# Optimization experiments

Hardware: AMD Instinct MI355X
Metric: run time of the kernel (lower is better)

The kernel has to match this reference:

```python
import jax, jax.numpy as jnp
import numpy as np

N_NODES = 50000
N_EDGES = 800000
IN_DIM = 128
HID = 32
HEADS = 4
OUT_DIM = 128
NEG_SLOPE = 0.2


def setup_inputs() -> dict:
    key = jax.random.key(0)
    ks = jax.random.split(key, 10)
    s = lambda fan_in: 1.0 / np.sqrt(fan_in)
    return {
        "x": jax.random.normal(ks[0], (N_NODES, IN_DIM), dtype=jnp.float32),
        "edge_index": jax.random.randint(ks[1], (2, N_EDGES), 0, N_NODES, dtype=jnp.int64),
        # encoder GATConv: in=IN_DIM, out=HID, heads=HEADS (concat)
        "W1": jax.random.normal(ks[2], (IN_DIM, HEADS * HID), dtype=jnp.float32) * s(IN_DIM),
        "att_src1": jax.random.normal(ks[3], (HEADS, HID), dtype=jnp.float32) * s(HID),
        "att_dst1": jax.random.normal(ks[4], (HEADS, HID), dtype=jnp.float32) * s(HID),
        "b1": jnp.zeros((HEADS * HID,), dtype=jnp.float32),
        # decoder GATConv: in=HEADS*HID, out=OUT_DIM, heads=1
        "W2": jax.random.normal(ks[5], (HEADS * HID, OUT_DIM), dtype=jnp.float32) * s(HEADS * HID),
        "att_src2": jax.random.normal(ks[6], (1, OUT_DIM), dtype=jnp.float32) * s(OUT_DIM),
        "att_dst2": jax.random.normal(ks[7], (1, OUT_DIM), dtype=jnp.float32) * s(OUT_DIM),
        "b2": jnp.zeros((OUT_DIM,), dtype=jnp.float32),
    }


def _gat_conv(x, src, dst, W, att_src, att_dst, bias, heads, out_ch):
    """PyG-style GATConv (v1), eval mode (dropout off), self-loops already in src/dst."""
    n = x.shape[0]
    h = (x @ W).reshape(n, heads, out_ch)                 # [N,H,C]
    a_src = jnp.einsum("nhc,hc->nh", h, att_src)          # [N,H]
    a_dst = jnp.einsum("nhc,hc->nh", h, att_dst)          # [N,H]
    e = jax.nn.leaky_relu(a_src[src] + a_dst[dst], NEG_SLOPE)  # [E,H]
    # segment softmax over destination neighborhoods
    e_max = jax.ops.segment_max(e, dst, num_segments=n)   # [N,H]
    e_exp = jnp.exp(e - e_max[dst])
    denom = jax.ops.segment_sum(e_exp, dst, num_segments=n)
    alpha = e_exp / (denom[dst] + 1e-16)                  # [E,H]
    msg = h[src] * alpha[:, :, None]                      # [E,H,C]
    out = jax.ops.segment_sum(msg, dst, num_segments=n)   # [N,H,C]
    return out.reshape(n, heads * out_ch) + bias


def reference(x, edge_index, W1, att_src1, att_dst1, b1, W2, att_src2, att_dst2, b2):
    n = x.shape[0]
    loops = jnp.arange(n, dtype=edge_index.dtype)
    src = jnp.concatenate([edge_index[0], loops])
    dst = jnp.concatenate([edge_index[1], loops])
    z = jax.nn.relu(_gat_conv(x, src, dst, W1, att_src1, att_dst1, b1, HEADS, HID))
    x_hat = jax.nn.relu(_gat_conv(z, src, dst, W2, att_src2, att_dst2, b2, 1, OUT_DIM))
    return x_hat
```

## Files before the change

### kernel.cpp

```cpp
#include <hip/hip_runtime.h>
#include <hip/hip_bf16.h>
#include <cstddef>

#define N_NODES 50000
#define N_EDGES_RAW 800000
#define E_TOT (N_EDGES_RAW + N_NODES)
#define DIM 128
#define NEG_SLOPE 0.2f

#define NBUCK 196
#define CHUNK 4096
#define NBLK_E ((E_TOT + CHUNK - 1) / CHUNK)

typedef __attribute__((ext_vector_type(8))) short bf16x8;
typedef __attribute__((ext_vector_type(4))) float f32x4;

__device__ __forceinline__ ushort f2bf(float f) {
  unsigned u = __float_as_uint(f);
  return (ushort)((u + 0x7FFFu + ((u >> 16) & 1u)) >> 16);
}

__device__ __forceinline__ void get_edge(const int* __restrict__ ei, int is64,
                                         int e, int& s, int& d) {
  if (e >= N_EDGES_RAW) { s = e - N_EDGES_RAW; d = s; return; }
  if (is64) {
    s = ei[2 * (size_t)e];
    d = ei[2 * ((size_t)N_EDGES_RAW + (size_t)e)];
  } else {
    s = ei[e];
    d = ei[N_EDGES_RAW + e];
  }
}

__device__ __forceinline__ int detect_inline(const int* __restrict__ ei,
                                             int* sflag) {
  const int t = threadIdx.x;
  if (t < 64) {
    int hi = ei[2 * t + 1];
    unsigned long long b = __ballot(hi != 0);
    if (t == 0) *sflag = (b == 0ULL) ? 1 : 0;
  }
  __syncthreads();
  return *sflag;
}

__device__ __forceinline__ void prep_one(const float* __restrict__ w,
                                         const float* __restrict__ atts,
                                         const float* __restrict__ attd,
                                         ushort* __restrict__ wtx,
                                         int H, int idx) {
  const int c = idx >> 7, k = idx & 127;
  const int C = 128 / H;
  float v;
  if (c < 128) {
    v = w[k * 128 + c];
  } else if (c < 128 + H) {
    const int hd = c - 128;
    float s = 0.f;
    for (int j = 0; j < C; ++j) s += w[k * 128 + hd * C + j] * atts[hd * C + j];
    v = s;
  } else if (c < 128 + 2 * H) {
    const int hd = c - 128 - H;
    float s = 0.f;
    for (int j = 0; j < C; ++j) s += w[k * 128 + hd * C + j] * attd[hd * C + j];
    v = s;
  } else {
    v = 0.f;
  }
  wtx[idx] = f2bf(v);
}

__global__ __launch_bounds__(256) void setup(const float* __restrict__ W1,
                                             const float* __restrict__ as1,
                                             const float* __restrict__ ad1,
                                             ushort* __restrict__ wtx1,
                                             const float* __restrict__ W2,
                                             const float* __restrict__ as2,
                                             const float* __restrict__ ad2,
                                             ushort* __restrict__ wtx2,
                                             int* __restrict__ gbcnt) {
  const int b = blockIdx.x, t = threadIdx.x;
  if (b < 72) {
    prep_one(W1, as1, ad1, wtx1, 4, b * 256 + t);
  } else if (b < 144) {
    prep_one(W2, as2, ad2, wtx2, 1, (b - 72) * 256 + t);
  } else {
    if (t < NBUCK) gbcnt[t] = 0;
  }
}

__global__ __launch_bounds__(256) void bucket_count(const int* __restrict__ ei,
                                                    int* __restrict__ gbcnt) {
  __shared__ int hist[NBUCK];
  __shared__ int sflag;
  const int t = threadIdx.x;
  if (t < NBUCK) hist[t] = 0;
  const int is64 = detect_inline(ei, &sflag);
  __syncthreads();
  const int e0 = blockIdx.x * CHUNK;
#pragma unroll
  for (int i = 0; i < CHUNK / 256; ++i) {
    int e = e0 + i * 256 + t;
    if (e < E_TOT) {
      int s, d;
      get_edge(ei, is64, e, s, d);
      atomicAdd(&hist[d >> 8], 1);
    }
  }
  __syncthreads();
  if (t < NBUCK && hist[t] > 0) atomicAdd(&gbcnt[t], hist[t]);
}

__global__ __launch_bounds__(256) void bucket_scan(const int* __restrict__ gbcnt,
                                                   int* __restrict__ bstart,
                                                   int* __restrict__ gcur) {
  __shared__ int wtot[4];
  const int t = threadIdx.x, lane = t & 63, wid = t >> 6;
  int v = (t < NBUCK) ? gbcnt[t] : 0;
  int sc = v;
#pragma unroll
  for (int m = 1; m < 64; m <<= 1) {
    int o = __shfl_up(sc, m, 64);
    if (lane >= m) sc += o;
  }
  if (lane == 63) wtot[wid] = sc;
  __syncthreads();
  int off = 0;
  for (int w = 0; w < wid; ++w) off += wtot[w];
  int excl = off + sc - v;
  if (t < NBUCK) {
    bstart[t] = excl;
    gcur[t] = excl;
  }
  if (t == 255) bstart[NBUCK] = off + sc;
}

__global__ __launch_bounds__(256) void bucket_scatter(const int* __restrict__ ei,
                                                      int* __restrict__ gcur,
                                                      unsigned* __restrict__ tmp) {
  __shared__ int hist[NBUCK];
  __shared__ int base[NBUCK];
  __shared__ int sflag;
  const int t = threadIdx.x;
  if (t < NBUCK) hist[t] = 0;
  const int is64 = detect_inline(ei, &sflag);
  __syncthreads();
  const int e0 = blockIdx.x * CHUNK;
  unsigned pair[CHUNK / 256];
  int rank[CHUNK / 256];
#pragma unroll
  for (int i = 0; i < CHUNK / 256; ++i) {
    int e = e0 + i * 256 + t;
    if (e < E_TOT) {
      int s, d;
      get_edge(ei, is64, e, s, d);
      pair[i] = (unsigned)s | ((unsigned)d << 16);
      rank[i] = atomicAdd(&hist[d >> 8], 1);
    }
  }
  __syncthreads();
  if (t < NBUCK && hist[t] > 0) base[t] = atomicAdd(&gcur[t], hist[t]);
  __syncthreads();
#pragma unroll
  for (int i = 0; i < CHUNK / 256; ++i) {
    int e = e0 + i * 256 + t;
    if (e < E_TOT) {
      int b = (int)(pair[i] >> 24);
      tmp[base[b] + rank[i]] = pair[i];
    }
  }
}

__global__ __launch_bounds__(256) void bucket_sort(const unsigned* __restrict__ tmp,
                                                   const int* __restrict__ bstart,
                                                   int* __restrict__ csr_src,
                                                   int* __restrict__ rp,
                                                   int* __restrict__ deg) {
  __shared__ int cnt[256];
  __shared__ int cur[256];
  __shared__ int wtot[4];
  const int b = blockIdx.x;
  const int t = threadIdx.x, lane = t & 63, wid = t >> 6;
  const int p0 = bstart[b], p1 = bstart[b + 1];
  cnt[t] = 0;
  __syncthreads();
  for (int j = p0 + t; j < p1; j += 256) {
    unsigned pr = tmp[j];
    atomicAdd(&cnt[(pr >> 16) & 255u], 1);
  }
  __syncthreads();
  int v = cnt[t];
  int sc = v;
#pragma unroll
  for (int m = 1; m < 64; m <<= 1) {
    int o = __shfl_up(sc, m, 64);
    if (lane >= m) sc += o;
  }
  if (lane == 63) wtot[wid] = sc;
  __syncthreads();
  int off = 0;
  for (int w = 0; w < wid; ++w) off += wtot[w];
  const int excl = off + sc - v;
  const int node = b * 256 + t;
  if (node < N_NODES) {
    deg[node] = v;
    rp[node] = p0 + excl;
  }
  cur[t] = excl;
  __syncthreads();
  for (int j = p0 + t; j < p1; j += 256) {
    unsigned pr = tmp[j];
    int ld = (int)((pr >> 16) & 255u);
    int r = atomicAdd(&cur[ld], 1);
    csr_src[p0 + r] = (int)(pr & 0xFFFFu);
  }
}

template <int H>
__global__ __launch_bounds__(256) void gemm_att(const float* __restrict__ in,
                                                const ushort* __restrict__ wtx,
                                                ushort* __restrict__ h_bf,
                                                float* __restrict__ a_src,
                                                float* __restrict__ a_dst) {
  const int wid = threadIdx.x >> 6;
  const int lane = threadIdx.x & 63;
  const int tile = blockIdx.x * 4 + wid;
  if (tile >= N_NODES / 16) return;
  const int row0 = tile * 16;
  const int rA = lane & 15;
  const int g = lane >> 4;

  f32x4 acc[9];
#pragma unroll
  for (int ct = 0; ct < 9; ++ct) acc[ct] = (f32x4){0.f, 0.f, 0.f, 0.f};

#pragma unroll
  for (int ks = 0; ks < 4; ++ks) {
    const int k0 = ks * 32 + g * 8;
    const float* ap = in + (size_t)(row0 + rA) * DIM + k0;
    float4 a0 = *(const float4*)ap;
    float4 a1 = *(const float4*)(ap + 4);
    bf16x8 af;
    af[0] = (short)f2bf(a0.x); af[1] = (short)f2bf(a0.y);
    af[2] = (short)f2bf(a0.z); af[3] = (short)f2bf(a0.w);
    af[4] = (short)f2bf(a1.x); af[5] = (short)f2bf(a1.y);
    af[6] = (short)f2bf(a1.z); af[7] = (short)f2bf(a1.w);
#pragma unroll
    for (int ct = 0; ct < 9; ++ct) {
      bf16x8 bf = *(const bf16x8*)(wtx + (size_t)(ct * 16 + rA) * 128 + k0);
      acc[ct] = __builtin_amdgcn_mfma_f32_16x16x32_bf16(af, bf, acc[ct], 0, 0, 0);
    }
  }

#pragma unroll
  for (int ct = 0; ct < 8; ++ct) {
#pragma unroll
    for (int r = 0; r < 4; ++r) {
      const int row = row0 + g * 4 + r;
      h_bf[(size_t)row * DIM + ct * 16 + rA] = f2bf(acc[ct][r]);
    }
  }
  if (rA < 2 * H) {
#pragma unroll
    for (int r = 0; r < 4; ++r) {
      const int row = row0 + g * 4 + r;
      if (rA < H)
        a_src[(size_t)row * H + rA] = acc[8][r];
      else
        a_dst[(size_t)row * H + (rA - H)] = acc[8][r];
    }
  }
}

template <int H>
__global__ __launch_bounds__(256) void node_agg(const int* __restrict__ rp,
                                                const int* __restrict__ deg,
                                                const int* __restrict__ csr_src,
                                                const ushort* __restrict__ h_bf,
                                                const float* __restrict__ a_src,
                                                const float* __restrict__ a_dst,
                                                const float* __restrict__ bias,
                                                float* __restrict__ outp) {
  const int wid = threadIdx.x >> 6;
  const int lane = threadIdx.x & 63;
  const int node = blockIdx.x * 4 + wid;
  if (node >= N_NODES) return;
  const int hl = lane & 31;
  const int head = (H == 4) ? (hl >> 3) : 0;
  const float ad = a_dst[(size_t)node * H + head];
  const int beg = rp[node];
  const int dg = deg[node];
  const int* __restrict__ srcs = csr_src + beg;

  float sden = 0.f;
  float a0 = 0.f, a1 = 0.f, a2 = 0.f, a3 = 0.f;

  const int dg2 = dg & ~1;
#pragma unroll 2
  for (int j = 0; j < dg2; j += 2) {
    int s = srcs[j + (lane >> 5)];
    float v = a_src[(size_t)s * H + head] + ad;
    v = v > 0.f ? v : NEG_SLOPE * v;
    v = fminf(fmaxf(v, -60.f), 80.f);
    float p = __expf(v);
    uint2 hv = ((const uint2*)(h_bf + (size_t)s * DIM))[hl];
    float h0 = __uint_as_float((hv.x & 0xFFFFu) << 16);
    float h1 = __uint_as_float(hv.x & 0xFFFF0000u);
    float h2 = __uint_as_float((hv.y & 0xFFFFu) << 16);
    float h3 = __uint_as_float(hv.y & 0xFFFF0000u);
    sden += p;
    a0 += p * h0; a1 += p * h1; a2 += p * h2; a3 += p * h3;
  }
  if (dg & 1) {
    int s = srcs[dg - 1];
    float v = a_src[(size_t)s * H + head] + ad;
    v = v > 0.f ? v : NEG_SLOPE * v;
    v = fminf(fmaxf(v, -60.f), 80.f);
    float p = __expf(v);
    if (lane >= 32) p = 0.f;
    uint2 hv = ((const uint2*)(h_bf + (size_t)s * DIM))[hl];
    float h0 = __uint_as_float((hv.x & 0xFFFFu) << 16);
    float h1 = __uint_as_float(hv.x & 0xFFFF0000u);
    float h2 = __uint_as_float((hv.y & 0xFFFFu) << 16);
    float h3 = __uint_as_float(hv.y & 0xFFFF0000u);
    sden += p;
    a0 += p * h0; a1 += p * h1; a2 += p * h2; a3 += p * h3;
  }

  sden += __shfl_xor(sden, 32);
  a0 += __shfl_xor(a0, 32);
  a1 += __shfl_xor(a1, 32);
  a2 += __shfl_xor(a2, 32);
  a3 += __shfl_xor(a3, 32);

  if (lane < 32) {
    const float inv = 1.f / sden;
    float4 bv = ((const float4*)bias)[hl];
    float4 o;
    o.x = fmaxf(a0 * inv + bv.x, 0.f);
    o.y = fmaxf(a1 * inv + bv.y, 0.f);
    o.z = fmaxf(a2 * inv + bv.z, 0.f);
    o.w = fmaxf(a3 * inv + bv.w, 0.f);
    ((float4*)(outp + (size_t)node * DIM))[hl] = o;
  }
}

extern "C" void kernel_launch(void* const* d_in, const int* in_sizes, int n_in,
                              void* d_out, int out_size, void* d_ws, size_t ws_size,
                              hipStream_t stream) {
  const float* x   = (const float*)d_in[0];
  const int*   ei  = (const int*)d_in[1];
  const float* W1  = (const float*)d_in[2];
  const float* as1 = (const float*)d_in[3];
  const float* ad1 = (const float*)d_in[4];
  const float* b1  = (const float*)d_in[5];
  const float* W2  = (const float*)d_in[6];
  const float* as2 = (const float*)d_in[7];
  const float* ad2 = (const float*)d_in[8];
  const float* b2  = (const float*)d_in[9];
  float* out = (float*)d_out;

  float* ws = (float*)d_ws;
  const size_t F_H = (size_t)N_NODES * DIM;
  float*    z      = ws;
  ushort*   h_bf   = (ushort*)(z + F_H);
  float*    a_src  = z + F_H + F_H / 2;
  float*    a_dst  = a_src + 200000;
  int*      deg    = (int*)(a_dst + 200000);
  int*      rp     = deg + N_NODES;
  int*      csr_src= rp + N_NODES;
  unsigned* tmp    = (unsigned*)(csr_src + E_TOT);
  int*      gbcnt  = (int*)(tmp + E_TOT);
  int*      bstart = gbcnt + 256;
  int*      gcur   = bstart + 256;
  ushort*   wtx1   = (ushort*)(gcur + 256);
  ushort*   wtx2   = wtx1 + 144 * 128;

  const int GB = (N_NODES / 16 + 3) / 4;

  hipLaunchKernelGGL(setup, dim3(145), dim3(256), 0, stream,
                     W1, as1, ad1, wtx1, W2, as2, ad2, wtx2, gbcnt);
  hipLaunchKernelGGL(bucket_count, dim3(NBLK_E), dim3(256), 0, stream, ei, gbcnt);
  hipLaunchKernelGGL(bucket_scan, dim3(1), dim3(256), 0, stream, gbcnt, bstart, gcur);
  hipLaunchKernelGGL(bucket_scatter, dim3(NBLK_E), dim3(256), 0, stream, ei, gcur, tmp);
  hipLaunchKernelGGL(bucket_sort, dim3(NBUCK), dim3(256), 0, stream,
                     tmp, bstart, csr_src, rp, deg);

  hipLaunchKernelGGL((gemm_att<4>), dim3(GB), dim3(256), 0, stream,
                     x, wtx1, h_bf, a_src, a_dst);
  hipLaunchKernelGGL((node_agg<4>), dim3((N_NODES + 3) / 4), dim3(256), 0, stream,
                     rp, deg, csr_src, h_bf, a_src, a_dst, b1, z);

  hipLaunchKernelGGL((gemm_att<1>), dim3(GB), dim3(256), 0, stream,
                     z, wtx2, h_bf, a_src, a_dst);
  hipLaunchKernelGGL((node_agg<1>), dim3((N_NODES + 3) / 4), dim3(256), 0, stream,
                     rp, deg, csr_src, h_bf, a_src, a_dst, b2, out);
}
```

Measured before the change: 178.3 us.

## Fuse setup kernels, store intermediates in bf16, widen per-lane aggregation loads

Setup, the fp32-to-bf16 conversion of x and the bucket histogram are merged into one launch. Per-block histograms are written to a matrix and summed in the scan kernel, which removes the global atomics and the zeroing step. The layer-1 output z is now stored as bf16, so the second GEMM reads half the bytes, and node aggregation handles 4 edges per wave with 16-byte loads and 8 accumulators per lane. In exchange, x is converted in a separate pass, and the scan kernel does a serial 208-block sum per bucket.

```diff
diff --git a/kernel.cpp b/kernel.cpp
--- a/kernel.cpp
+++ b/kernel.cpp
@@ -11,6 +11,7 @@
 #define NBUCK 196
 #define CHUNK 4096
 #define NBLK_E ((E_TOT + CHUNK - 1) / CHUNK)
+#define CONV_BLKS 3125
 
 typedef __attribute__((ext_vector_type(8))) short bf16x8;
 typedef __attribute__((ext_vector_type(4))) float f32x4;
@@ -18,6 +19,12 @@
 __device__ __forceinline__ ushort f2bf(float f) {
   unsigned u = __float_as_uint(f);
   return (ushort)((u + 0x7FFFu + ((u >> 16) & 1u)) >> 16);
+}
+__device__ __forceinline__ float bf2f_lo(uint u) {
+  return __uint_as_float(u << 16);
+}
+__device__ __forceinline__ float bf2f_hi(uint u) {
+  return __uint_as_float(u & 0xFFFF0000u);
 }
 
 __device__ __forceinline__ void get_edge(const int* __restrict__ ei, int is64,
@@ -70,53 +77,56 @@
   wtx[idx] = f2bf(v);
 }
 
-__global__ __launch_bounds__(256) void setup(const float* __restrict__ W1,
-                                             const float* __restrict__ as1,
-                                             const float* __restrict__ ad1,
-                                             ushort* __restrict__ wtx1,
-                                             const float* __restrict__ W2,
-                                             const float* __restrict__ as2,
-                                             const float* __restrict__ ad2,
-                                             ushort* __restrict__ wtx2,
-                                             int* __restrict__ gbcnt) {
+__global__ __launch_bounds__(256) void mega_setup(
+    const float* __restrict__ W1, const float* __restrict__ as1,
+    const float* __restrict__ ad1, ushort* __restrict__ wtx1,
+    const float* __restrict__ W2, const float* __restrict__ as2,
+    const float* __restrict__ ad2, ushort* __restrict__ wtx2,
+    const float* __restrict__ x, ushort* __restrict__ x_bf,
+    const int* __restrict__ ei, int* __restrict__ hist_mat) {
   const int b = blockIdx.x, t = threadIdx.x;
   if (b < 72) {
     prep_one(W1, as1, ad1, wtx1, 4, b * 256 + t);
   } else if (b < 144) {
     prep_one(W2, as2, ad2, wtx2, 1, (b - 72) * 256 + t);
+  } else if (b < 144 + CONV_BLKS) {
+    const int base = (b - 144) * 2048 + t * 8;
+    float4 v0 = *(const float4*)(x + base);
+    float4 v1 = *(const float4*)(x + base + 4);
+    ushort u[8];
+    u[0] = f2bf(v0.x); u[1] = f2bf(v0.y); u[2] = f2bf(v0.z); u[3] = f2bf(v0.w);
+    u[4] = f2bf(v1.x); u[5] = f2bf(v1.y); u[6] = f2bf(v1.z); u[7] = f2bf(v1.w);
+    *(uint4*)(x_bf + base) = *(const uint4*)u;
   } else {
-    if (t < NBUCK) gbcnt[t] = 0;
-  }
-}
-
-__global__ __launch_bounds__(256) void bucket_count(const int* __restrict__ ei,
-                                                    int* __restrict__ gbcnt) {
-  __shared__ int hist[NBUCK];
-  __shared__ int sflag;
-  const int t = threadIdx.x;
-  if (t < NBUCK) hist[t] = 0;
-  const int is64 = detect_inline(ei, &sflag);
-  __syncthreads();
-  const int e0 = blockIdx.x * CHUNK;
-#pragma unroll
-  for (int i = 0; i < CHUNK / 256; ++i) {
-    int e = e0 + i * 256 + t;
-    if (e < E_TOT) {
-      int s, d;
-      get_edge(ei, is64, e, s, d);
-      atomicAdd(&hist[d >> 8], 1);
-    }
-  }
-  __syncthreads();
-  if (t < NBUCK && hist[t] > 0) atomicAdd(&gbcnt[t], hist[t]);
-}
-
-__global__ __launch_bounds__(256) void bucket_scan(const int* __restrict__ gbcnt,
+    __shared__ int hist[NBUCK];
+    __shared__ int sflag;
+    const int cb = b - 144 - CONV_BLKS;
+    if (t < NBUCK) hist[t] = 0;
+    const int is64 = detect_inline(ei, &sflag);
+    __syncthreads();
+    const int e0 = cb * CHUNK;
+#pragma unroll
+    for (int i = 0; i < CHUNK / 256; ++i) {
+      int e = e0 + i * 256 + t;
+      if (e < E_TOT) {
+        int s, d;
+        get_edge(ei, is64, e, s, d);
+        atomicAdd(&hist[d >> 8], 1);
+      }
+    }
+    __syncthreads();
+    if (t < NBUCK) hist_mat[cb * NBUCK + t] = hist[t];
+  }
+}
+
+__global__ __launch_bounds__(256) void bucket_scan(const int* __restrict__ hist_mat,
                                                    int* __restrict__ bstart,
                                                    int* __restrict__ gcur) {
   __shared__ int wtot[4];
   const int t = threadIdx.x, lane = t & 63, wid = t >> 6;
-  int v = (t < NBUCK) ? gbcnt[t] : 0;
+  int v = 0;
+  if (t < NBUCK)
+    for (int b = 0; b < NBLK_E; ++b) v += hist_mat[b * NBUCK + t];
   int sc = v;
 #pragma unroll
   for (int m = 1; m < 64; m <<= 1) {
@@ -217,7 +227,7 @@
 }
 
 template <int H>
-__global__ __launch_bounds__(256) void gemm_att(const float* __restrict__ in,
+__global__ __launch_bounds__(256) void gemm_att(const ushort* __restrict__ in_bf,
                                                 const ushort* __restrict__ wtx,
                                                 ushort* __restrict__ h_bf,
                                                 float* __restrict__ a_src,
@@ -237,14 +247,7 @@
 #pragma unroll
   for (int ks = 0; ks < 4; ++ks) {
     const int k0 = ks * 32 + g * 8;
-    const float* ap = in + (size_t)(row0 + rA) * DIM + k0;
-    float4 a0 = *(const float4*)ap;
-    float4 a1 = *(const float4*)(ap + 4);
-    bf16x8 af;
-    af[0] = (short)f2bf(a0.x); af[1] = (short)f2bf(a0.y);
-    af[2] = (short)f2bf(a0.z); af[3] = (short)f2bf(a0.w);
-    af[4] = (short)f2bf(a1.x); af[5] = (short)f2bf(a1.y);
-    af[6] = (short)f2bf(a1.z); af[7] = (short)f2bf(a1.w);
+    bf16x8 af = *(const bf16x8*)(in_bf + (size_t)(row0 + rA) * DIM + k0);
 #pragma unroll
     for (int ct = 0; ct < 9; ++ct) {
       bf16x8 bf = *(const bf16x8*)(wtx + (size_t)(ct * 16 + rA) * 128 + k0);
@@ -272,7 +275,7 @@
   }
 }
 
-template <int H>
+template <int H, bool OBF>
 __global__ __launch_bounds__(256) void node_agg(const int* __restrict__ rp,
                                                 const int* __restrict__ deg,
                                                 const int* __restrict__ csr_src,
@@ -280,13 +283,14 @@
                                                 const float* __restrict__ a_src,
                                                 const float* __restrict__ a_dst,
                                                 const float* __restrict__ bias,
-                                                float* __restrict__ outp) {
+                                                void* __restrict__ outp) {
   const int wid = threadIdx.x >> 6;
   const int lane = threadIdx.x & 63;
   const int node = blockIdx.x * 4 + wid;
   if (node >= N_NODES) return;
-  const int hl = lane & 31;
-  const int head = (H == 4) ? (hl >> 3) : 0;
+  const int ql = lane >> 4;
+  const int hl = lane & 15;
+  const int head = (H == 4) ? (hl >> 2) : 0;
   const float ad = a_dst[(size_t)node * H + head];
   const int beg = rp[node];
   const int dg = deg[node];
@@ -294,54 +298,68 @@
 
   float sden = 0.f;
   float a0 = 0.f, a1 = 0.f, a2 = 0.f, a3 = 0.f;
-
-  const int dg2 = dg & ~1;
+  float a4 = 0.f, a5 = 0.f, a6 = 0.f, a7 = 0.f;
+
+  int j = 0;
 #pragma unroll 2
-  for (int j = 0; j < dg2; j += 2) {
-    int s = srcs[j + (lane >> 5)];
+  for (; j + 4 <= dg; j += 4) {
+    int s = srcs[j + ql];
     float v = a_src[(size_t)s * H + head] + ad;
     v = v > 0.f ? v : NEG_SLOPE * v;
     v = fminf(fmaxf(v, -60.f), 80.f);
     float p = __expf(v);
-    uint2 hv = ((const uint2*)(h_bf + (size_t)s * DIM))[hl];
-    float h0 = __uint_as_float((hv.x & 0xFFFFu) << 16);
-    float h1 = __uint_as_float(hv.x & 0xFFFF0000u);
-    float h2 = __uint_as_float((hv.y & 0xFFFFu) << 16);
-    float h3 = __uint_as_float(hv.y & 0xFFFF0000u);
+    uint4 hv = ((const uint4*)(h_bf + (size_t)s * DIM))[hl];
     sden += p;
-    a0 += p * h0; a1 += p * h1; a2 += p * h2; a3 += p * h3;
-  }
-  if (dg & 1) {
-    int s = srcs[dg - 1];
+    a0 += p * bf2f_lo(hv.x); a1 += p * bf2f_hi(hv.x);
+    a2 += p * bf2f_lo(hv.y); a3 += p * bf2f_hi(hv.y);
+    a4 += p * bf2f_lo(hv.z); a5 += p * bf2f_hi(hv.z);
+    a6 += p * bf2f_lo(hv.w); a7 += p * bf2f_hi(hv.w);
+  }
+  if (j < dg) {
+    int jj = j + ql;
+    int s = srcs[jj < dg ? jj : (dg - 1)];
     float v = a_src[(size_t)s * H + head] + ad;
     v = v > 0.f ? v : NEG_SLOPE * v;
     v = fminf(fmaxf(v, -60.f), 80.f);
-    float p = __expf(v);
-    if (lane >= 32) p = 0.f;
-    uint2 hv = ((const uint2*)(h_bf + (size_t)s * DIM))[hl];
-    float h0 = __uint_as_float((hv.x & 0xFFFFu) << 16);
-    float h1 = __uint_as_float(hv.x & 0xFFFF0000u);
-    float h2 = __uint_as_float((hv.y & 0xFFFFu) << 16);
-    float h3 = __uint_as_float(hv.y & 0xFFFF0000u);
+    float p = (jj < dg) ? __expf(v) : 0.f;
+    uint4 hv = ((const uint4*)(h_bf + (size_t)s * DIM))[hl];
     sden += p;
-    a0 += p * h0; a1 += p * h1; a2 += p * h2; a3 += p * h3;
-  }
-
-  sden += __shfl_xor(sden, 32);
-  a0 += __shfl_xor(a0, 32);
-  a1 += __shfl_xor(a1, 32);
-  a2 += __shfl_xor(a2, 32);
-  a3 += __shfl_xor(a3, 32);
-
-  if (lane < 32) {
+    a0 += p * bf2f_lo(hv.x); a1 += p * bf2f_hi(hv.x);
+    a2 += p * bf2f_lo(hv.y); a3 += p * bf2f_hi(hv.y);
+    a4 += p * bf2f_lo(hv.z); a5 += p * bf2f_hi(hv.z);
+    a6 += p * bf2f_lo(hv.w); a7 += p * bf2f_hi(hv.w);
+  }
+
+#pragma unroll
+  for (int m = 32; m >= 16; m >>= 1) {
+    sden += __shfl_xor(sden, m);
+    a0 += __shfl_xor(a0, m); a1 += __shfl_xor(a1, m);
+    a2 += __shfl_xor(a2, m); a3 += __shfl_xor(a3, m);
+    a4 += __shfl_xor(a4, m); a5 += __shfl_xor(a5, m);
+    a6 += __shfl_xor(a6, m); a7 += __shfl_xor(a7, m);
+  }
+
+  if (lane < 16) {
     const float inv = 1.f / sden;
-    float4 bv = ((const float4*)bias)[hl];
-    float4 o;
-    o.x = fmaxf(a0 * inv + bv.x, 0.f);
-    o.y = fmaxf(a1 * inv + bv.y, 0.f);
-    o.z = fmaxf(a2 * inv + bv.z, 0.f);
-    o.w = fmaxf(a3 * inv + bv.w, 0.f);
-    ((float4*)(outp + (size_t)node * DIM))[hl] = o;
+    float4 bv0 = ((const float4*)bias)[2 * hl];
+    float4 bv1 = ((const float4*)bias)[2 * hl + 1];
+    float o0 = fmaxf(a0 * inv + bv0.x, 0.f);
+    float o1 = fmaxf(a1 * inv + bv0.y, 0.f);
+    float o2 = fmaxf(a2 * inv + bv0.z, 0.f);
+    float o3 = fmaxf(a3 * inv + bv0.w, 0.f);
+    float o4 = fmaxf(a4 * inv + bv1.x, 0.f);
+    float o5 = fmaxf(a5 * inv + bv1.y, 0.f);
+    float o6 = fmaxf(a6 * inv + bv1.z, 0.f);
+    float o7 = fmaxf(a7 * inv + bv1.w, 0.f);
+    if (OBF) {
+      ushort u[8] = {f2bf(o0), f2bf(o1), f2bf(o2), f2bf(o3),
+                     f2bf(o4), f2bf(o5), f2bf(o6), f2bf(o7)};
+      ((uint4*)((ushort*)outp + (size_t)node * DIM))[hl] = *(const uint4*)u;
+    } else {
+      float* op = (float*)outp + (size_t)node * DIM;
+      ((float4*)op)[2 * hl] = make_float4(o0, o1, o2, o3);
+      ((float4*)op)[2 * hl + 1] = make_float4(o4, o5, o6, o7);
+    }
   }
 }
 
@@ -360,39 +378,42 @@
   const float* b2  = (const float*)d_in[9];
   float* out = (float*)d_out;
 
-  float* ws = (float*)d_ws;
+  char* ws = (char*)d_ws;
   const size_t F_H = (size_t)N_NODES * DIM;
-  float*    z      = ws;
-  ushort*   h_bf   = (ushort*)(z + F_H);
-  float*    a_src  = z + F_H + F_H / 2;
-  float*    a_dst  = a_src + 200000;
-  int*      deg    = (int*)(a_dst + 200000);
-  int*      rp     = deg + N_NODES;
-  int*      csr_src= rp + N_NODES;
-  unsigned* tmp    = (unsigned*)(csr_src + E_TOT);
-  int*      gbcnt  = (int*)(tmp + E_TOT);
-  int*      bstart = gbcnt + 256;
-  int*      gcur   = bstart + 256;
-  ushort*   wtx1   = (ushort*)(gcur + 256);
-  ushort*   wtx2   = wtx1 + 144 * 128;
+  ushort* h_bf    = (ushort*)ws;
+  ushort* z_bf    = h_bf + F_H;
+  ushort* x_bf    = z_bf + F_H;
+  float*  a_src   = (float*)(x_bf + F_H);
+  float*  a_dst   = a_src + 200000;
+  int*    deg     = (int*)(a_dst + 200000);
+  int*    rp      = deg + N_NODES;
+  int*    csr_src = rp + N_NODES;
+  unsigned* tmp   = (unsigned*)(csr_src + E_TOT);
+  int*    hist_mat= (int*)(tmp + E_TOT);
+  int*    bstart  = hist_mat + NBLK_E * NBUCK;
+  int*    gcur    = bstart + NBUCK + 1;
+  ushort* wtx1    = (ushort*)(gcur + NBUCK + 3);
+  ushort* wtx2    = wtx1 + 144 * 128;
 
   const int GB = (N_NODES / 16 + 3) / 4;
-
-  hipLaunchKernelGGL(setup, dim3(145), dim3(256), 0, stream,
-                     W1, as1, ad1, wtx1, W2, as2, ad2, wtx2, gbcnt);
-  hipLaunchKernelGGL(bucket_count, dim3(NBLK_E), dim3(256), 0, stream, ei, gbcnt);
-  hipLaunchKernelGGL(bucket_scan, dim3(1), dim3(256), 0, stream, gbcnt, bstart, gcur);
-  hipLaunchKernelGGL(bucket_scatter, dim3(NBLK_E), dim3(256), 0, stream, ei, gcur, tmp);
+  const int MEGA = 144 + CONV_BLKS + NBLK_E;
+
+  hipLaunchKernelGGL(mega_setup, dim3(MEGA), dim3(256), 0, stream,
+                     W1, as1, ad1, wtx1, W2, as2, ad2, wtx2, x, x_bf, ei, hist_mat);
+  hipLaunchKernelGGL(bucket_scan, dim3(1), dim3(256), 0, stream,
+                     hist_mat, bstart, gcur);
+  hipLaunchKernelGGL(bucket_scatter, dim3(NBLK_E), dim3(256), 0, stream,
+                     ei, gcur, tmp);
   hipLaunchKernelGGL(bucket_sort, dim3(NBUCK), dim3(256), 0, stream,
                      tmp, bstart, csr_src, rp, deg);
 
   hipLaunchKernelGGL((gemm_att<4>), dim3(GB), dim3(256), 0, stream,
-                     x, wtx1, h_bf, a_src, a_dst);
-  hipLaunchKernelGGL((node_agg<4>), dim3((N_NODES + 3) / 4), dim3(256), 0, stream,
-                     rp, deg, csr_src, h_bf, a_src, a_dst, b1, z);
+                     x_bf, wtx1, h_bf, a_src, a_dst);
+  hipLaunchKernelGGL((node_agg<4, true>), dim3((N_NODES + 3) / 4), dim3(256), 0,
+                     stream, rp, deg, csr_src, h_bf, a_src, a_dst, b1, z_bf);
 
   hipLaunchKernelGGL((gemm_att<1>), dim3(GB), dim3(256), 0, stream,
-                     z, wtx2, h_bf, a_src, a_dst);
-  hipLaunchKernelGGL((node_agg<1>), dim3((N_NODES + 3) / 4), dim3(256), 0, stream,
-                     rp, deg, csr_src, h_bf, a_src, a_dst, b2, out);
-}
+                     z_bf, wtx2, h_bf, a_src, a_dst);
+  hipLaunchKernelGGL((node_agg<1, false>), dim3((N_NODES + 3) / 4), dim3(256), 0,
+                     stream, rp, deg, csr_src, h_bf, a_src, a_dst, b2, out);
+}
```

After: 169.6 us. 1.05x faster.
